# Kernel tuning notes

Hardware: AMD Instinct MI355X
Metric: run time of the kernel (lower is better)

The kernel has to match this reference:

```python
import jax, jax.numpy as jnp
import numpy as np

B, N, DIM, HEADS, DEPTH, MLP = 4, 1024, 256, 4, 4, 1024
DH = DIM // HEADS
EPS = 1e-5


def _ln(x, g, b):
    mu = jnp.mean(x, axis=-1, keepdims=True)
    var = jnp.mean((x - mu) ** 2, axis=-1, keepdims=True)
    return (x - mu) / jnp.sqrt(var + EPS) * g + b


def setup_inputs() -> dict:
    key = jax.random.key(0)
    ks = jax.random.split(key, 10)
    s = 0.02
    p = {}
    p["x"] = jax.random.normal(ks[0], (B, N, DIM), jnp.float32)
    p["attn_bias"] = jax.random.normal(ks[1], (2, B, HEADS, N, N), jnp.float32)
    p["ln1_g"] = jnp.ones((DEPTH, DIM), jnp.float32)
    p["ln1_b"] = jnp.zeros((DEPTH, DIM), jnp.float32)
    p["Wkv"] = jax.random.normal(ks[2], (DEPTH, DIM, 2 * DIM), jnp.float32) * s
    p["Wq"] = jax.random.normal(ks[3], (DEPTH, DIM, DIM), jnp.float32) * s
    p["Wo"] = jax.random.normal(ks[4], (DEPTH, DIM, DIM), jnp.float32) * s
    p["bo"] = jnp.zeros((DEPTH, DIM), jnp.float32)
    p["ln2_g"] = jnp.ones((DEPTH, DIM), jnp.float32)
    p["ln2_b"] = jnp.zeros((DEPTH, DIM), jnp.float32)
    p["W1"] = jax.random.normal(ks[5], (DEPTH, DIM, MLP), jnp.float32) * s
    p["b1"] = jnp.zeros((DEPTH, MLP), jnp.float32)
    p["W2"] = jax.random.normal(ks[6], (DEPTH, MLP, DIM), jnp.float32) * s
    p["b2"] = jnp.zeros((DEPTH, DIM), jnp.float32)
    p["Wg"] = jax.random.normal(ks[7], (DIM, DIM), jnp.float32) * s
    p["lng_g"] = jnp.ones((DIM,), jnp.float32)
    p["lng_b"] = jnp.zeros((DIM,), jnp.float32)
    return p


def reference(x, attn_bias, ln1_g, ln1_b, Wkv, Wq, Wo, bo, ln2_g, ln2_b, W1, b1, W2, b2, Wg, lng_g, lng_b):
    scale = DIM ** -0.5
    add_attn = attn_bias[0] + attn_bias[1]            # [B,H,N,N]
    # aggregation bias matrices are layer-invariant (recomputed identically each layer in torch)
    A = jnp.mean(attn_bias[0], axis=1)                # [B,N,N]
    S = jnp.mean(attn_bias[1], axis=1)
    G = jax.nn.softmax(A * S, axis=2)                 # [B,N,N]

    def split_heads(t):  # [B,N,DIM] -> [B,H,N,DH]
        return t.reshape(B, N, HEADS, DH).transpose(0, 2, 1, 3)

    for l in range(DEPTH):
        # softmax-GCN aggregation
        x_ma = jax.nn.relu(_ln(jnp.matmul(G, x) @ Wg, lng_g, lng_b))
        # attention (PreNorm on x only; q comes from un-normed x_ma)
        xn = _ln(x, ln1_g[l], ln1_b[l])
        kv = xn @ Wkv[l]
        k, v = jnp.split(kv, 2, axis=-1)
        q = x_ma @ Wq[l]
        qh, kh, vh = split_heads(q), split_heads(k), split_heads(v)
        dots = jnp.einsum('bhid,bhjd->bhij', qh, kh) * scale + add_attn
        attn = jax.nn.softmax(dots, axis=-1)
        out = jnp.einsum('bhij,bhjd->bhid', attn, vh)
        out = out.transpose(0, 2, 1, 3).reshape(B, N, DIM)
        x = x + out @ Wo[l] + bo[l]
        # feed-forward (exact GELU, matching torch nn.GELU default)
        xn2 = _ln(x, ln2_g[l], ln2_b[l])
        x = x + jax.nn.gelu(xn2 @ W1[l] + b1[l], approximate=False) @ W2[l] + b2[l]
    return x
```

## Files before the change

kernel.cpp:

```cpp
#include <hip/hip_runtime.h>
#include <hip/hip_bf16.h>
#include <math.h>

typedef unsigned short u16;
typedef __bf16 bf16x8 __attribute__((ext_vector_type(8)));
typedef float f32x4 __attribute__((ext_vector_type(4)));

#define B_ 4
#define N_ 1024
#define DIM_ 256
#define HEADS_ 4
#define DH_ 64
#define MLP_ 1024
#define DEPTH_ 4

__device__ __forceinline__ float r2f(u16 r){ return __uint_as_float(((unsigned)r)<<16); }
__device__ __forceinline__ u16 f2r(float f){ __hip_bfloat16 h = __float2bfloat16(f); return *(u16*)&h; }

__device__ __forceinline__ float gelu_exact(float v){
  return 0.5f*v*(1.0f + erff(v*0.70710678118654752440f));
}

#define MFMA16(a,b,c) __builtin_amdgcn_mfma_f32_16x16x32_bf16(a,b,c,0,0,0)

__global__ void prep_bias(const float* __restrict__ bias, u16* __restrict__ G, u16* __restrict__ bsum){
  int blk = blockIdx.x;
  int i = blk & (N_-1);
  int b = blk >> 10;
  int t = threadIdx.x;
  __shared__ float red[256];
  long long base0 = ((long long)(b*HEADS_)*N_ + i)*(long long)N_;
  const long long hs = (long long)N_*N_;
  const long long cs = (long long)B_*HEADS_*N_*N_;
  int j0 = t*4;
  f32x4 a = {0.f,0.f,0.f,0.f}, s = {0.f,0.f,0.f,0.f};
  #pragma unroll
  for (int h=0;h<HEADS_;h++){
    f32x4 x0 = *(const f32x4*)(bias + base0 + h*hs + j0);
    f32x4 x1 = *(const f32x4*)(bias + cs + base0 + h*hs + j0);
    a += x0; s += x1;
    union { ushort4 u; u16 e[4]; } pk;
    #pragma unroll
    for (int k=0;k<4;k++) pk.e[k] = f2r(x0[k]+x1[k]);
    *(ushort4*)(bsum + base0 + h*hs + j0) = pk.u;
  }
  float v[4]; float lmax = -3e38f;
  #pragma unroll
  for (int k=0;k<4;k++){ v[k] = (a[k]*0.25f)*(s[k]*0.25f); lmax = fmaxf(lmax, v[k]); }
  red[t]=lmax; __syncthreads();
  for (int st=128;st>0;st>>=1){ if(t<st) red[t]=fmaxf(red[t],red[t+st]); __syncthreads(); }
  float m = red[0]; __syncthreads();
  float e[4]; float lsum = 0.f;
  #pragma unroll
  for (int k=0;k<4;k++){ e[k] = __expf(v[k]-m); lsum += e[k]; }
  red[t]=lsum; __syncthreads();
  for (int st=128;st>0;st>>=1){ if(t<st) red[t]+=red[t+st]; __syncthreads(); }
  float inv = 1.0f/red[0];
  u16* Grow = G + ((long long)b*N_ + i)*(long long)N_;
  union { ushort4 u; u16 e[4]; } pg;
  #pragma unroll
  for (int k=0;k<4;k++) pg.e[k] = f2r(e[k]*inv);
  *(ushort4*)(Grow + j0) = pg.u;
}

__global__ void ln_kernel(const float* __restrict__ X, u16* __restrict__ Y,
                          const float* __restrict__ g, const float* __restrict__ bvec){
  int row = blockIdx.x*8 + (threadIdx.x>>5);
  int cg = threadIdx.x&31;
  const float* xp = X + (long long)row*DIM_ + cg*8;
  f32x4 v0 = *(const f32x4*)xp;
  f32x4 v1 = *(const f32x4*)(xp+4);
  float s = v0[0]+v0[1]+v0[2]+v0[3]+v1[0]+v1[1]+v1[2]+v1[3];
  s += __shfl_xor(s,1); s += __shfl_xor(s,2); s += __shfl_xor(s,4); s += __shfl_xor(s,8); s += __shfl_xor(s,16);
  float mu = s*(1.0f/256.0f);
  float s2 = 0.f;
  #pragma unroll
  for (int k=0;k<4;k++){ float d=v0[k]-mu; s2 += d*d; }
  #pragma unroll
  for (int k=0;k<4;k++){ float d=v1[k]-mu; s2 += d*d; }
  s2 += __shfl_xor(s2,1); s2 += __shfl_xor(s2,2); s2 += __shfl_xor(s2,4); s2 += __shfl_xor(s2,8); s2 += __shfl_xor(s2,16);
  float rstd = rsqrtf(s2*(1.0f/256.0f)+1e-5f);
  f32x4 g0 = *(const f32x4*)(g + cg*8);
  f32x4 g1 = *(const f32x4*)(g + cg*8 + 4);
  f32x4 b0 = *(const f32x4*)(bvec + cg*8);
  f32x4 b1 = *(const f32x4*)(bvec + cg*8 + 4);
  union { ushort4 u[2]; u16 e[8]; } pk;
  #pragma unroll
  for (int k=0;k<4;k++) pk.e[k]   = f2r((v0[k]-mu)*rstd*g0[k] + b0[k]);
  #pragma unroll
  for (int k=0;k<4;k++) pk.e[4+k] = f2r((v1[k]-mu)*rstd*g1[k] + b1[k]);
  u16* yp = Y + (long long)row*DIM_ + cg*8;
  *(ushort4*)yp = pk.u[0];
  *(ushort4*)(yp+4) = pk.u[1];
}

__global__ void tcast_all(const float* __restrict__ Wkv, const float* __restrict__ Wq,
                          const float* __restrict__ Wo, const float* __restrict__ W1,
                          const float* __restrict__ W2, const float* __restrict__ Wg,
                          const float* __restrict__ xin,
                          u16* WkvT, u16* WqT, u16* WoT, u16* W1T, u16* W2T, u16* WgT, u16* xT){
  int z = blockIdx.z;
  const float* I; u16* O; int ldin, R, C;
  if (z < 4)       { I = Wkv + z*131072;      O = WkvT + z*131072;      ldin=512;  R=256;  C=512;  }
  else if (z < 8)  { I = Wq  + (z-4)*65536;   O = WqT  + (z-4)*65536;   ldin=256;  R=256;  C=256;  }
  else if (z < 12) { I = Wo  + (z-8)*65536;   O = WoT  + (z-8)*65536;   ldin=256;  R=256;  C=256;  }
  else if (z < 16) { I = W1  + (z-12)*262144; O = W1T  + (z-12)*262144; ldin=1024; R=256;  C=1024; }
  else if (z < 20) { I = W2  + (z-16)*262144; O = W2T  + (z-16)*262144; ldin=256;  R=1024; C=256;  }
  else if (z == 20){ I = Wg;                  O = WgT;                  ldin=256;  R=256;  C=256;  }
  else             { I = xin + (z-21)*262144; O = xT   + (z-21)*262144; ldin=256;  R=1024; C=256;  }
  int c0 = blockIdx.x*32, r0 = blockIdx.y*32;
  if (c0 >= C || r0 >= R) return;
  __shared__ float tile[32][33];
  int tx = threadIdx.x, ty = threadIdx.y;
  #pragma unroll
  for (int i=0;i<4;i++)
    tile[ty*4+i][tx] = I[(long long)(r0+ty*4+i)*ldin + c0+tx];
  __syncthreads();
  #pragma unroll
  for (int i=0;i<4;i++)
    O[(long long)(c0+ty*4+i)*R + r0+tx] = f2r(tile[tx][ty*4+i]);
}

__global__ __launch_bounds__(512, 4) void layer_pre(
    const u16* __restrict__ Gb, const u16* __restrict__ xT, const u16* __restrict__ xnb,
    const u16* __restrict__ WgT, const u16* __restrict__ WqT, const u16* __restrict__ WkvT,
    const float* __restrict__ lng, const float* __restrict__ lnb,
    u16* __restrict__ qb, u16* __restrict__ kvb, u16* __restrict__ vt)
{
  __shared__ float Gx_s[16][264];
  __shared__ float t2_s[16][264];
  __shared__ u16  xma_s[16][264];
  int tid = threadIdx.x;
  int w = tid>>6, lane = tid&63, lr = lane&15, qd = lane>>4;
  int bid = blockIdx.x;

  if (bid >= 256){
    int row0 = (bid-256)*16;
    int batch = row0>>10;
    const u16* Ap = xnb + (long long)(row0+lr)*DIM_;
    f32x4 acc[4] = {};
    for (int k0=0;k0<256;k0+=32){
      bf16x8 af = *(const bf16x8*)(Ap + k0 + qd*8);
      #pragma unroll
      for (int i=0;i<4;i++){
        bf16x8 bf = *(const bf16x8*)(WkvT + (long long)((w*4+i)*16+lr)*256 + k0 + qd*8);
        acc[i] = MFMA16(af,bf,acc[i]);
      }
    }
    #pragma unroll
    for (int i=0;i<4;i++){
      int col = (w*4+i)*16+lr;
      #pragma unroll
      for (int r=0;r<4;r++){
        int row = row0+qd*4+r;
        float v = acc[i][r];
        kvb[(long long)row*512 + col] = f2r(v);
        if (col >= 256)
          vt[(long long)batch*262144 + (long long)(col-256)*1024 + (row&1023)] = f2r(v);
      }
    }
    return;
  }

  int row0 = bid*16;
  int batch = row0>>10, brow0 = row0&1023;

  {
    int kw = w>>2, cw = w&3;
    const u16* Ap = Gb + (long long)batch*1048576 + (long long)(brow0+lr)*1024 + kw*512;
    const u16* Bp = xT + (long long)batch*262144 + (long long)kw*512;
    f32x4 acc[4] = {};
    for (int k0=0;k0<512;k0+=32){
      bf16x8 af = *(const bf16x8*)(Ap + k0 + qd*8);
      #pragma unroll
      for (int nt=0;nt<4;nt++){
        bf16x8 bf = *(const bf16x8*)(Bp + (long long)(cw*64+nt*16+lr)*1024 + k0 + qd*8);
        acc[nt] = MFMA16(af,bf,acc[nt]);
      }
    }
    if (kw==0){
      #pragma unroll
      for (int nt=0;nt<4;nt++)
        #pragma unroll
        for (int r=0;r<4;r++) Gx_s[qd*4+r][cw*64+nt*16+lr] = acc[nt][r];
    }
    __syncthreads();
    if (kw==1){
      #pragma unroll
      for (int nt=0;nt<4;nt++)
        #pragma unroll
        for (int r=0;r<4;r++) Gx_s[qd*4+r][cw*64+nt*16+lr] += acc[nt][r];
    }
    __syncthreads();
  }
  {
    int r = tid>>5, cg2 = tid&31;
    #pragma unroll
    for (int i=0;i<8;i++) xma_s[r][cg2*8+i] = f2r(Gx_s[r][cg2*8+i]);
  }
  __syncthreads();
  {
    f32x4 acc[2] = {};
    for (int k0=0;k0<256;k0+=32){
      bf16x8 af = *(const bf16x8*)&xma_s[lr][k0+qd*8];
      #pragma unroll
      for (int i=0;i<2;i++){
        bf16x8 bf = *(const bf16x8*)(WgT + (long long)((w*2+i)*16+lr)*256 + k0 + qd*8);
        acc[i] = MFMA16(af,bf,acc[i]);
      }
    }
    #pragma unroll
    for (int i=0;i<2;i++)
      #pragma unroll
      for (int r=0;r<4;r++) t2_s[qd*4+r][(w*2+i)*16+lr] = acc[i][r];
  }
  __syncthreads();
  {
    int r = tid>>5, cg2 = tid&31;
    float v[8]; float s=0.f;
    #pragma unroll
    for (int i=0;i<8;i++){ v[i] = t2_s[r][cg2*8+i]; s += v[i]; }
    s += __shfl_xor(s,1); s += __shfl_xor(s,2); s += __shfl_xor(s,4); s += __shfl_xor(s,8); s += __shfl_xor(s,16);
    float mu = s*(1.0f/256.0f);
    float s2=0.f;
    #pragma unroll
    for (int i=0;i<8;i++){ float d=v[i]-mu; s2 += d*d; }
    s2 += __shfl_xor(s2,1); s2 += __shfl_xor(s2,2); s2 += __shfl_xor(s2,4); s2 += __shfl_xor(s2,8); s2 += __shfl_xor(s2,16);
    float rstd = rsqrtf(s2*(1.0f/256.0f)+1e-5f);
    #pragma unroll
    for (int i=0;i<8;i++){
      int c = cg2*8+i;
      float y = (v[i]-mu)*rstd*lng[c] + lnb[c];
      xma_s[r][c] = f2r(fmaxf(y,0.f));
    }
  }
  __syncthreads();
  {
    f32x4 acc[2] = {};
    for (int k0=0;k0<256;k0+=32){
      bf16x8 af = *(const bf16x8*)&xma_s[lr][k0+qd*8];
      #pragma unroll
      for (int i=0;i<2;i++){
        bf16x8 bf = *(const bf16x8*)(WqT + (long long)((w*2+i)*16+lr)*256 + k0 + qd*8);
        acc[i] = MFMA16(af,bf,acc[i]);
      }
    }
    #pragma unroll
    for (int i=0;i<2;i++)
      #pragma unroll
      for (int r=0;r<4;r++)
        qb[(long long)(row0+qd*4+r)*DIM_ + (w*2+i)*16+lr] = f2r(acc[i][r]);
  }
}

#define APSMEM 72704
__global__ __launch_bounds__(512, 2) void attn_post(
    const u16* __restrict__ qb, const u16* __restrict__ kvb,
    const u16* __restrict__ vt, const u16* __restrict__ bsum,
    const float* __restrict__ resx,
    const u16* __restrict__ WoT, const float* __restrict__ bo,
    const float* __restrict__ ln2g, const float* __restrict__ ln2b,
    const u16* __restrict__ W1T, const float* __restrict__ b1,
    const u16* __restrict__ W2T, const float* __restrict__ b2,
    float* __restrict__ xf_out,
    const float* __restrict__ ln1g_next, const float* __restrict__ ln1b_next,
    u16* __restrict__ xn_out, u16* __restrict__ xT_out)
{
  __shared__ __align__(16) char smem[APSMEM];
  u16 (*sb)[16][72]   = (u16 (*)[16][72])smem;
  u16 (*Pl)[16][72]   = (u16 (*)[16][72])(smem+18432);
  float (*Ol)[16][68] = (float(*)[16][68])(smem+36864);
  float (*Ml)[16]     = (float(*)[16])(smem+71680);
  float (*Ll)[16]     = (float(*)[16])(smem+72192);
  u16  (*ao_s)[264]   = (u16 (*)[264])smem;
  float (*v_s)[264]   = (float(*)[264])(smem+8448);
  u16  (*xn2_s)[264]  = (u16 (*)[264])(smem+25344);
  u16  (*h1_s)[1048]  = (u16 (*)[1048])(smem+33792);
  float (*xnew_s)[264]= (float(*)[264])(smem+33792);

  int tid = threadIdx.x;
  int w = tid>>6, lane = tid&63, lr = lane&15, qd = lane>>4;
  int row0 = blockIdx.x*16;
  int batch = row0>>10, brow0 = row0&1023;

  {
    int h = w>>1, g = w&1;
    int z = batch*HEADS_ + h;
    const u16* qp = qb + ((long long)row0 + lr)*DIM_ + h*DH_;
    bf16x8 aq0 = *(const bf16x8*)(qp + qd*8);
    bf16x8 aq1 = *(const bf16x8*)(qp + 32 + qd*8);

    f32x4 oacc[4] = {};
    float m_r[4] = {-3e38f,-3e38f,-3e38f,-3e38f};
    float l_r[4] = {0.f,0.f,0.f,0.f};

    const u16* kbase = kvb + ((long long)(batch*N_))*512 + h*DH_;
    const u16* vbase = vt + (long long)batch*(DIM_*N_) + (long long)(h*DH_)*N_;
    const u16* bias_base = bsum + ((long long)z*N_ + brow0)*(long long)N_;
    int srr = lane>>2, scc = (lane&3)*16;

    for (int jtl=0; jtl<8; jtl++){
      int j0 = (g*8 + jtl)*64;
      {
        const u16* gs = bias_base + (long long)srr*N_ + j0 + scc;
        uint4 t0 = *(const uint4*)gs;
        uint4 t1 = *(const uint4*)(gs+8);
        *(uint4*)&sb[w][srr][scc]   = t0;
        *(uint4*)&sb[w][srr][scc+8] = t1;
      }
      f32x4 sacc[4] = {};
      #pragma unroll
      for (int nt=0; nt<4; nt++){
        const u16* kp = kbase + (long long)(j0 + nt*16 + lr)*512;
        bf16x8 bk0 = *(const bf16x8*)(kp + qd*8);
        bf16x8 bk1 = *(const bf16x8*)(kp + 32 + qd*8);
        sacc[nt] = MFMA16(aq0, bk0, sacc[nt]);
        sacc[nt] = MFMA16(aq1, bk1, sacc[nt]);
      }
      #pragma unroll
      for (int r=0;r<4;r++){
        float pv[4];
        float vmax = -3e38f;
        #pragma unroll
        for (int nt=0;nt<4;nt++){
          float v = sacc[nt][r]*0.0625f + r2f(sb[w][qd*4+r][nt*16+lr]);
          pv[nt] = v;
          vmax = fmaxf(vmax, v);
        }
        vmax = fmaxf(vmax, __shfl_xor(vmax,1));
        vmax = fmaxf(vmax, __shfl_xor(vmax,2));
        vmax = fmaxf(vmax, __shfl_xor(vmax,4));
        vmax = fmaxf(vmax, __shfl_xor(vmax,8));
        float newm = fmaxf(m_r[r], vmax);
        float alpha = __expf(m_r[r]-newm);
        m_r[r] = newm;
        float psum = 0.f;
        #pragma unroll
        for (int nt=0;nt<4;nt++){
          float p = __expf(pv[nt]-newm);
          psum += p;
          Pl[w][qd*4+r][nt*16+lr] = f2r(p);
        }
        psum += __shfl_xor(psum,1);
        psum += __shfl_xor(psum,2);
        psum += __shfl_xor(psum,4);
        psum += __shfl_xor(psum,8);
        l_r[r] = l_r[r]*alpha + psum;
        #pragma unroll
        for (int ot=0;ot<4;ot++) oacc[ot][r] *= alpha;
      }
      #pragma unroll
      for (int ks=0;ks<2;ks++){
        bf16x8 ap = *(const bf16x8*)&Pl[w][lr][ks*32 + qd*8];
        #pragma unroll
        for (int ot=0;ot<4;ot++){
          const u16* vp = vbase + (long long)(ot*16+lr)*N_ + j0 + ks*32 + qd*8;
          bf16x8 bv = *(const bf16x8*)vp;
          oacc[ot] = MFMA16(ap, bv, oacc[ot]);
        }
      }
    }
    #pragma unroll
    for (int r=0;r<4;r++){
      int row = qd*4+r;
      #pragma unroll
      for (int ot=0;ot<4;ot++) Ol[w][row][ot*16+lr] = oacc[ot][r];
      if (lr==0){ Ml[w][row] = m_r[r]; Ll[w][row] = l_r[r]; }
    }
  }
  __syncthreads();
  if (!(w&1)){
    int h = w>>1;
    #pragma unroll
    for (int r=0;r<4;r++){
      int row = qd*4+r;
      float m0 = Ml[w][row], m1 = Ml[w+1][row];
      float mm = fmaxf(m0,m1);
      float e0 = __expf(m0-mm), e1 = __expf(m1-mm);
      float inv = 1.0f/(Ll[w][row]*e0 + Ll[w+1][row]*e1);
      #pragma unroll
      for (int ot=0;ot<4;ot++){
        float o = Ol[w][row][ot*16+lr]*e0 + Ol[w+1][row][ot*16+lr]*e1;
        ao_s[row][h*DH_ + ot*16+lr] = f2r(o*inv);
      }
    }
  }
  __syncthreads();

  {
    f32x4 acc[2] = {};
    for (int k0=0;k0<256;k0+=32){
      bf16x8 af = *(const bf16x8*)&ao_s[lr][k0+qd*8];
      #pragma unroll
      for (int i=0;i<2;i++){
        bf16x8 bf = *(const bf16x8*)(WoT + (long long)((w*2+i)*16+lr)*256 + k0 + qd*8);
        acc[i] = MFMA16(af,bf,acc[i]);
      }
    }
    #pragma unroll
    for (int i=0;i<2;i++){
      int col = (w*2+i)*16+lr;
      #pragma unroll
      for (int r=0;r<4;r++)
        v_s[qd*4+r][col] = acc[i][r] + bo[col] + resx[(long long)(row0+qd*4+r)*DIM_ + col];
    }
  }
  __syncthreads();
  {
    int r = tid>>5, cg2 = tid&31;
    float v[8]; float s=0.f;
    #pragma unroll
    for (int i=0;i<8;i++){ v[i] = v_s[r][cg2*8+i]; s += v[i]; }
    s += __shfl_xor(s,1); s += __shfl_xor(s,2); s += __shfl_xor(s,4); s += __shfl_xor(s,8); s += __shfl_xor(s,16);
    float mu = s*(1.0f/256.0f);
    float s2=0.f;
    #pragma unroll
    for (int i=0;i<8;i++){ float d=v[i]-mu; s2 += d*d; }
    s2 += __shfl_xor(s2,1); s2 += __shfl_xor(s2,2); s2 += __shfl_xor(s2,4); s2 += __shfl_xor(s2,8); s2 += __shfl_xor(s2,16);
    float rstd = rsqrtf(s2*(1.0f/256.0f)+1e-5f);
    #pragma unroll
    for (int i=0;i<8;i++){
      int c = cg2*8+i;
      xn2_s[r][c] = f2r((v[i]-mu)*rstd*ln2g[c] + ln2b[c]);
    }
  }
  __syncthreads();
  {
    f32x4 acc[8] = {};
    for (int k0=0;k0<256;k0+=32){
      bf16x8 af = *(const bf16x8*)&xn2_s[lr][k0+qd*8];
      #pragma unroll
      for (int i=0;i<8;i++){
        bf16x8 bf = *(const bf16x8*)(W1T + (long long)((w*8+i)*16+lr)*256 + k0 + qd*8);
        acc[i] = MFMA16(af,bf,acc[i]);
      }
    }
    #pragma unroll
    for (int i=0;i<8;i++){
      int col = (w*8+i)*16+lr;
      #pragma unroll
      for (int r=0;r<4;r++)
        h1_s[qd*4+r][col] = f2r(gelu_exact(acc[i][r] + b1[col]));
    }
  }
  __syncthreads();
  {
    f32x4 acc[2] = {};
    for (int k0=0;k0<1024;k0+=32){
      bf16x8 af = *(const bf16x8*)&h1_s[lr][k0+qd*8];
      #pragma unroll
      for (int i=0;i<2;i++){
        bf16x8 bf = *(const bf16x8*)(W2T + (long long)((w*2+i)*16+lr)*1024 + k0 + qd*8);
        acc[i] = MFMA16(af,bf,acc[i]);
      }
    }
    __syncthreads();
    #pragma unroll
    for (int i=0;i<2;i++){
      int col = (w*2+i)*16+lr;
      #pragma unroll
      for (int r=0;r<4;r++){
        float v = acc[i][r] + b2[col] + v_s[qd*4+r][col];
        xf_out[(long long)(row0+qd*4+r)*DIM_ + col] = v;
        xnew_s[qd*4+r][col] = v;
      }
    }
  }
  if (ln1g_next){
    __syncthreads();
    int r = tid>>5, cg2 = tid&31;
    float v[8]; float s=0.f;
    #pragma unroll
    for (int i=0;i<8;i++){ v[i] = xnew_s[r][cg2*8+i]; s += v[i]; }
    s += __shfl_xor(s,1); s += __shfl_xor(s,2); s += __shfl_xor(s,4); s += __shfl_xor(s,8); s += __shfl_xor(s,16);
    float mu = s*(1.0f/256.0f);
    float s2=0.f;
    #pragma unroll
    for (int i=0;i<8;i++){ float d=v[i]-mu; s2 += d*d; }
    s2 += __shfl_xor(s2,1); s2 += __shfl_xor(s2,2); s2 += __shfl_xor(s2,4); s2 += __shfl_xor(s2,8); s2 += __shfl_xor(s2,16);
    float rstd = rsqrtf(s2*(1.0f/256.0f)+1e-5f);
    int grow = row0 + r;
    #pragma unroll
    for (int i=0;i<8;i++){
      int c = cg2*8+i;
      xn_out[(long long)grow*DIM_ + c] = f2r((v[i]-mu)*rstd*ln1g_next[c] + ln1b_next[c]);
      xT_out[(long long)batch*262144 + (long long)c*1024 + ((grow)&1023)] = f2r(v[i]);
    }
  }
}

extern "C" void kernel_launch(void* const* d_in, const int* in_sizes, int n_in,
                              void* d_out, int out_size, void* d_ws, size_t ws_size,
                              hipStream_t stream){
  const float* x_in   = (const float*)d_in[0];
  const float* abias  = (const float*)d_in[1];
  const float* ln1_g  = (const float*)d_in[2];
  const float* ln1_b  = (const float*)d_in[3];
  const float* Wkv    = (const float*)d_in[4];
  const float* Wq     = (const float*)d_in[5];
  const float* Wo     = (const float*)d_in[6];
  const float* bo     = (const float*)d_in[7];
  const float* ln2_g  = (const float*)d_in[8];
  const float* ln2_b  = (const float*)d_in[9];
  const float* W1     = (const float*)d_in[10];
  const float* b1     = (const float*)d_in[11];
  const float* W2     = (const float*)d_in[12];
  const float* b2     = (const float*)d_in[13];
  const float* Wg     = (const float*)d_in[14];
  const float* lng_g  = (const float*)d_in[15];
  const float* lng_b  = (const float*)d_in[16];

  char* ws = (char*)d_ws;
  float* xf   = (float*)(ws);
  u16*  Gb    = (u16*)(ws + (4ll<<20));
  u16*  bsum  = (u16*)(ws + (12ll<<20));
  u16*  kvb   = (u16*)(ws + (44ll<<20));
  u16*  vt    = (u16*)(ws + (48ll<<20));
  u16*  xT    = (u16*)(ws + (50ll<<20));
  u16*  xnb   = (u16*)(ws + (52ll<<20));
  u16*  qb    = (u16*)(ws + (54ll<<20));
  u16*  WkvT  = (u16*)(ws + (58ll<<20));
  u16*  WqT   = (u16*)(ws + (59ll<<20));
  u16*  WoT   = (u16*)(ws + (59ll<<20) + (512ll<<10));
  u16*  W1T   = (u16*)(ws + (60ll<<20));
  u16*  W2T   = (u16*)(ws + (62ll<<20));
  u16*  WgT   = (u16*)(ws + (64ll<<20));

  prep_bias<<<dim3(B_*N_), dim3(256), 0, stream>>>(abias, Gb, bsum);
  tcast_all<<<dim3(32,32,25), dim3(32,8), 0, stream>>>(Wkv,Wq,Wo,W1,W2,Wg,x_in,
                                                       WkvT,WqT,WoT,W1T,W2T,WgT,xT);
  ln_kernel<<<dim3(512), dim3(256), 0, stream>>>(x_in, xnb, ln1_g, ln1_b);

  for (int l=0; l<DEPTH_; l++){
    const float* resx = (l==0) ? x_in : xf;
    layer_pre<<<dim3(512), dim3(512), 0, stream>>>(Gb, xT, xnb,
        WgT, WqT + (long long)l*65536, WkvT + (long long)l*131072,
        lng_g, lng_b, qb, kvb, vt);
    if (l < DEPTH_-1){
      attn_post<<<dim3(256), dim3(512), 0, stream>>>(qb, kvb, vt, bsum, resx,
          WoT + (long long)l*65536, bo + l*DIM_, ln2_g + l*DIM_, ln2_b + l*DIM_,
          W1T + (long long)l*262144, b1 + l*MLP_, W2T + (long long)l*262144, b2 + l*DIM_,
          xf, ln1_g + (l+1)*DIM_, ln1_b + (l+1)*DIM_, xnb, xT);
    } else {
      attn_post<<<dim3(256), dim3(512), 0, stream>>>(qb, kvb, vt, bsum, resx,
          WoT + (long long)l*65536, bo + l*DIM_, ln2_g + l*DIM_, ln2_b + l*DIM_,
          W1T + (long long)l*262144, b1 + l*MLP_, W2T + (long long)l*262144, b2 + l*DIM_,
          (float*)d_out, nullptr, nullptr, nullptr, nullptr);
    }
  }
}
```

Measured before the change: 737.1 us.

## Halve attn_post row tile to 8 rows and fuse prep_bias with first LayerNorm

attn_post now handles 8 query rows per block instead of 16, so the grid doubles to 512 blocks and launch_bounds asks for 4 blocks per SM. It still fills the 16-row MFMA tiles by duplicating rows (index &7) and masks the writes to the first 8 rows. The aim is better CU occupancy and load balance on the attention+MLP stage. The cost is that half of the MFMA work and all Wo/W1/W2 weight reads per row are duplicated. Separately, prep_bias and the initial ln_kernel are merged into one launch to save one kernel launch.

```diff
diff --git a/kernel.cpp b/kernel.cpp
--- a/kernel.cpp
+++ b/kernel.cpp
@@ -23,75 +23,76 @@
 
 #define MFMA16(a,b,c) __builtin_amdgcn_mfma_f32_16x16x32_bf16(a,b,c,0,0,0)
 
-__global__ void prep_bias(const float* __restrict__ bias, u16* __restrict__ G, u16* __restrict__ bsum){
-  int blk = blockIdx.x;
-  int i = blk & (N_-1);
-  int b = blk >> 10;
-  int t = threadIdx.x;
-  __shared__ float red[256];
-  long long base0 = ((long long)(b*HEADS_)*N_ + i)*(long long)N_;
-  const long long hs = (long long)N_*N_;
-  const long long cs = (long long)B_*HEADS_*N_*N_;
-  int j0 = t*4;
-  f32x4 a = {0.f,0.f,0.f,0.f}, s = {0.f,0.f,0.f,0.f};
-  #pragma unroll
-  for (int h=0;h<HEADS_;h++){
-    f32x4 x0 = *(const f32x4*)(bias + base0 + h*hs + j0);
-    f32x4 x1 = *(const f32x4*)(bias + cs + base0 + h*hs + j0);
-    a += x0; s += x1;
-    union { ushort4 u; u16 e[4]; } pk;
-    #pragma unroll
-    for (int k=0;k<4;k++) pk.e[k] = f2r(x0[k]+x1[k]);
-    *(ushort4*)(bsum + base0 + h*hs + j0) = pk.u;
-  }
-  float v[4]; float lmax = -3e38f;
-  #pragma unroll
-  for (int k=0;k<4;k++){ v[k] = (a[k]*0.25f)*(s[k]*0.25f); lmax = fmaxf(lmax, v[k]); }
-  red[t]=lmax; __syncthreads();
-  for (int st=128;st>0;st>>=1){ if(t<st) red[t]=fmaxf(red[t],red[t+st]); __syncthreads(); }
-  float m = red[0]; __syncthreads();
-  float e[4]; float lsum = 0.f;
-  #pragma unroll
-  for (int k=0;k<4;k++){ e[k] = __expf(v[k]-m); lsum += e[k]; }
-  red[t]=lsum; __syncthreads();
-  for (int st=128;st>0;st>>=1){ if(t<st) red[t]+=red[t+st]; __syncthreads(); }
-  float inv = 1.0f/red[0];
-  u16* Grow = G + ((long long)b*N_ + i)*(long long)N_;
-  union { ushort4 u; u16 e[4]; } pg;
-  #pragma unroll
-  for (int k=0;k<4;k++) pg.e[k] = f2r(e[k]*inv);
-  *(ushort4*)(Grow + j0) = pg.u;
-}
-
-__global__ void ln_kernel(const float* __restrict__ X, u16* __restrict__ Y,
-                          const float* __restrict__ g, const float* __restrict__ bvec){
-  int row = blockIdx.x*8 + (threadIdx.x>>5);
-  int cg = threadIdx.x&31;
-  const float* xp = X + (long long)row*DIM_ + cg*8;
-  f32x4 v0 = *(const f32x4*)xp;
-  f32x4 v1 = *(const f32x4*)(xp+4);
-  float s = v0[0]+v0[1]+v0[2]+v0[3]+v1[0]+v1[1]+v1[2]+v1[3];
-  s += __shfl_xor(s,1); s += __shfl_xor(s,2); s += __shfl_xor(s,4); s += __shfl_xor(s,8); s += __shfl_xor(s,16);
-  float mu = s*(1.0f/256.0f);
-  float s2 = 0.f;
-  #pragma unroll
-  for (int k=0;k<4;k++){ float d=v0[k]-mu; s2 += d*d; }
-  #pragma unroll
-  for (int k=0;k<4;k++){ float d=v1[k]-mu; s2 += d*d; }
-  s2 += __shfl_xor(s2,1); s2 += __shfl_xor(s2,2); s2 += __shfl_xor(s2,4); s2 += __shfl_xor(s2,8); s2 += __shfl_xor(s2,16);
-  float rstd = rsqrtf(s2*(1.0f/256.0f)+1e-5f);
-  f32x4 g0 = *(const f32x4*)(g + cg*8);
-  f32x4 g1 = *(const f32x4*)(g + cg*8 + 4);
-  f32x4 b0 = *(const f32x4*)(bvec + cg*8);
-  f32x4 b1 = *(const f32x4*)(bvec + cg*8 + 4);
-  union { ushort4 u[2]; u16 e[8]; } pk;
-  #pragma unroll
-  for (int k=0;k<4;k++) pk.e[k]   = f2r((v0[k]-mu)*rstd*g0[k] + b0[k]);
-  #pragma unroll
-  for (int k=0;k<4;k++) pk.e[4+k] = f2r((v1[k]-mu)*rstd*g1[k] + b1[k]);
-  u16* yp = Y + (long long)row*DIM_ + cg*8;
-  *(ushort4*)yp = pk.u[0];
-  *(ushort4*)(yp+4) = pk.u[1];
+__global__ void prep_fused(const float* __restrict__ bias, u16* __restrict__ G, u16* __restrict__ bsum,
+                           const float* __restrict__ X, u16* __restrict__ Y,
+                           const float* __restrict__ g, const float* __restrict__ bvec){
+  if (blockIdx.x < 4096){
+    int blk = blockIdx.x;
+    int i = blk & (N_-1);
+    int b = blk >> 10;
+    int t = threadIdx.x;
+    __shared__ float red[256];
+    long long base0 = ((long long)(b*HEADS_)*N_ + i)*(long long)N_;
+    const long long hs = (long long)N_*N_;
+    const long long cs = (long long)B_*HEADS_*N_*N_;
+    int j0 = t*4;
+    f32x4 a = {0.f,0.f,0.f,0.f}, s = {0.f,0.f,0.f,0.f};
+    #pragma unroll
+    for (int h=0;h<HEADS_;h++){
+      f32x4 x0 = *(const f32x4*)(bias + base0 + h*hs + j0);
+      f32x4 x1 = *(const f32x4*)(bias + cs + base0 + h*hs + j0);
+      a += x0; s += x1;
+      union { ushort4 u; u16 e[4]; } pk;
+      #pragma unroll
+      for (int k=0;k<4;k++) pk.e[k] = f2r(x0[k]+x1[k]);
+      *(ushort4*)(bsum + base0 + h*hs + j0) = pk.u;
+    }
+    float v[4]; float lmax = -3e38f;
+    #pragma unroll
+    for (int k=0;k<4;k++){ v[k] = (a[k]*0.25f)*(s[k]*0.25f); lmax = fmaxf(lmax, v[k]); }
+    red[t]=lmax; __syncthreads();
+    for (int st=128;st>0;st>>=1){ if(t<st) red[t]=fmaxf(red[t],red[t+st]); __syncthreads(); }
+    float m = red[0]; __syncthreads();
+    float e[4]; float lsum = 0.f;
+    #pragma unroll
+    for (int k=0;k<4;k++){ e[k] = __expf(v[k]-m); lsum += e[k]; }
+    red[t]=lsum; __syncthreads();
+    for (int st=128;st>0;st>>=1){ if(t<st) red[t]+=red[t+st]; __syncthreads(); }
+    float inv = 1.0f/red[0];
+    u16* Grow = G + ((long long)b*N_ + i)*(long long)N_;
+    union { ushort4 u; u16 e[4]; } pg;
+    #pragma unroll
+    for (int k=0;k<4;k++) pg.e[k] = f2r(e[k]*inv);
+    *(ushort4*)(Grow + j0) = pg.u;
+  } else {
+    int row = (blockIdx.x-4096)*8 + (threadIdx.x>>5);
+    int cg = threadIdx.x&31;
+    const float* xp = X + (long long)row*DIM_ + cg*8;
+    f32x4 v0 = *(const f32x4*)xp;
+    f32x4 v1 = *(const f32x4*)(xp+4);
+    float s = v0[0]+v0[1]+v0[2]+v0[3]+v1[0]+v1[1]+v1[2]+v1[3];
+    s += __shfl_xor(s,1); s += __shfl_xor(s,2); s += __shfl_xor(s,4); s += __shfl_xor(s,8); s += __shfl_xor(s,16);
+    float mu = s*(1.0f/256.0f);
+    float s2 = 0.f;
+    #pragma unroll
+    for (int k=0;k<4;k++){ float d=v0[k]-mu; s2 += d*d; }
+    #pragma unroll
+    for (int k=0;k<4;k++){ float d=v1[k]-mu; s2 += d*d; }
+    s2 += __shfl_xor(s2,1); s2 += __shfl_xor(s2,2); s2 += __shfl_xor(s2,4); s2 += __shfl_xor(s2,8); s2 += __shfl_xor(s2,16);
+    float rstd = rsqrtf(s2*(1.0f/256.0f)+1e-5f);
+    f32x4 g0 = *(const f32x4*)(g + cg*8);
+    f32x4 g1 = *(const f32x4*)(g + cg*8 + 4);
+    f32x4 b0 = *(const f32x4*)(bvec + cg*8);
+    f32x4 b1 = *(const f32x4*)(bvec + cg*8 + 4);
+    union { ushort4 u[2]; u16 e[8]; } pk;
+    #pragma unroll
+    for (int k=0;k<4;k++) pk.e[k]   = f2r((v0[k]-mu)*rstd*g0[k] + b0[k]);
+    #pragma unroll
+    for (int k=0;k<4;k++) pk.e[4+k] = f2r((v1[k]-mu)*rstd*g1[k] + b1[k]);
+    u16* yp = Y + (long long)row*DIM_ + cg*8;
+    *(ushort4*)yp = pk.u[0];
+    *(ushort4*)(yp+4) = pk.u[1];
+  }
 }
 
 __global__ void tcast_all(const float* __restrict__ Wkv, const float* __restrict__ Wq,
@@ -254,7 +255,7 @@
 }
 
 #define APSMEM 72704
-__global__ __launch_bounds__(512, 2) void attn_post(
+__global__ __launch_bounds__(512, 4) void attn_post(
     const u16* __restrict__ qb, const u16* __restrict__ kvb,
     const u16* __restrict__ vt, const u16* __restrict__ bsum,
     const float* __restrict__ resx,
@@ -280,13 +281,13 @@
 
   int tid = threadIdx.x;
   int w = tid>>6, lane = tid&63, lr = lane&15, qd = lane>>4;
-  int row0 = blockIdx.x*16;
+  int row0 = blockIdx.x*8;
   int batch = row0>>10, brow0 = row0&1023;
 
   {
     int h = w>>1, g = w&1;
     int z = batch*HEADS_ + h;
-    const u16* qp = qb + ((long long)row0 + lr)*DIM_ + h*DH_;
+    const u16* qp = qb + ((long long)row0 + (lr&7))*DIM_ + h*DH_;
     bf16x8 aq0 = *(const bf16x8*)(qp + qd*8);
     bf16x8 aq1 = *(const bf16x8*)(qp + 32 + qd*8);
 
@@ -302,7 +303,7 @@
     for (int jtl=0; jtl<8; jtl++){
       int j0 = (g*8 + jtl)*64;
       {
-        const u16* gs = bias_base + (long long)srr*N_ + j0 + scc;
+        const u16* gs = bias_base + (long long)(srr&7)*N_ + j0 + scc;
         uint4 t0 = *(const uint4*)gs;
         uint4 t1 = *(const uint4*)(gs+8);
         *(uint4*)&sb[w][srr][scc]   = t0;
@@ -402,7 +403,8 @@
       int col = (w*2+i)*16+lr;
       #pragma unroll
       for (int r=0;r<4;r++)
-        v_s[qd*4+r][col] = acc[i][r] + bo[col] + resx[(long long)(row0+qd*4+r)*DIM_ + col];
+        v_s[qd*4+r][col] = acc[i][r] + bo[col]
+                         + resx[(long long)(row0+((qd*4+r)&7))*DIM_ + col];
     }
   }
   __syncthreads();
@@ -460,9 +462,11 @@
       int col = (w*2+i)*16+lr;
       #pragma unroll
       for (int r=0;r<4;r++){
-        float v = acc[i][r] + b2[col] + v_s[qd*4+r][col];
-        xf_out[(long long)(row0+qd*4+r)*DIM_ + col] = v;
-        xnew_s[qd*4+r][col] = v;
+        int row = qd*4+r;
+        float v = acc[i][r] + b2[col] + v_s[row][col];
+        if (row < 8)
+          xf_out[(long long)(row0+row)*DIM_ + col] = v;
+        xnew_s[row][col] = v;
       }
     }
   }
@@ -479,12 +483,14 @@
     for (int i=0;i<8;i++){ float d=v[i]-mu; s2 += d*d; }
     s2 += __shfl_xor(s2,1); s2 += __shfl_xor(s2,2); s2 += __shfl_xor(s2,4); s2 += __shfl_xor(s2,8); s2 += __shfl_xor(s2,16);
     float rstd = rsqrtf(s2*(1.0f/256.0f)+1e-5f);
-    int grow = row0 + r;
-    #pragma unroll
-    for (int i=0;i<8;i++){
-      int c = cg2*8+i;
-      xn_out[(long long)grow*DIM_ + c] = f2r((v[i]-mu)*rstd*ln1g_next[c] + ln1b_next[c]);
-      xT_out[(long long)batch*262144 + (long long)c*1024 + ((grow)&1023)] = f2r(v[i]);
+    if (r < 8){
+      int grow = row0 + r;
+      #pragma unroll
+      for (int i=0;i<8;i++){
+        int c = cg2*8+i;
+        xn_out[(long long)grow*DIM_ + c] = f2r((v[i]-mu)*rstd*ln1g_next[c] + ln1b_next[c]);
+        xT_out[(long long)batch*262144 + (long long)c*1024 + (grow&1023)] = f2r(v[i]);
+      }
     }
   }
 }
@@ -526,10 +532,9 @@
   u16*  W2T   = (u16*)(ws + (62ll<<20));
   u16*  WgT   = (u16*)(ws + (64ll<<20));
 
-  prep_bias<<<dim3(B_*N_), dim3(256), 0, stream>>>(abias, Gb, bsum);
+  prep_fused<<<dim3(4608), dim3(256), 0, stream>>>(abias, Gb, bsum, x_in, xnb, ln1_g, ln1_b);
   tcast_all<<<dim3(32,32,25), dim3(32,8), 0, stream>>>(Wkv,Wq,Wo,W1,W2,Wg,x_in,
                                                        WkvT,WqT,WoT,W1T,W2T,WgT,xT);
-  ln_kernel<<<dim3(512), dim3(256), 0, stream>>>(x_in, xnb, ln1_g, ln1_b);
 
   for (int l=0; l<DEPTH_; l++){
     const float* resx = (l==0) ? x_in : xf;
@@ -537,12 +542,12 @@
         WgT, WqT + (long long)l*65536, WkvT + (long long)l*131072,
         lng_g, lng_b, qb, kvb, vt);
     if (l < DEPTH_-1){
-      attn_post<<<dim3(256), dim3(512), 0, stream>>>(qb, kvb, vt, bsum, resx,
+      attn_post<<<dim3(512), dim3(512), 0, stream>>>(qb, kvb, vt, bsum, resx,
           WoT + (long long)l*65536, bo + l*DIM_, ln2_g + l*DIM_, ln2_b + l*DIM_,
           W1T + (long long)l*262144, b1 + l*MLP_, W2T + (long long)l*262144, b2 + l*DIM_,
           xf, ln1_g + (l+1)*DIM_, ln1_b + (l+1)*DIM_, xnb, xT);
     } else {
-      attn_post<<<dim3(256), dim3(512), 0, stream>>>(qb, kvb, vt, bsum, resx,
+      attn_post<<<dim3(512), dim3(512), 0, stream>>>(qb, kvb, vt, bsum, resx,
           WoT + (long long)l*65536, bo + l*DIM_, ln2_g + l*DIM_, ln2_b + l*DIM_,
           W1T + (long long)l*262144, b1 + l*MLP_, W2T + (long long)l*262144, b2 + l*DIM_,
           (float*)d_out, nullptr, nullptr, nullptr, nullptr);
```

Result: slower. 922.7 us (+25.2%).
